# Kernel tuning notes

Measured on AMD Instinct MI355X. Metric: run time of the kernel, lower is better.

Reference implementation:

```python
import jax, jax.numpy as jnp
import numpy as np
import math

N, D, H = 4096, 2048, 16
HD = D // H  # head_dim = 128


def setup_inputs() -> dict:
    key = jax.random.key(0)
    ks = jax.random.split(key, 9)
    s = 1.0 / math.sqrt(D)
    return {
        "x":  jax.random.normal(ks[0], (N, D), dtype=jnp.float32),
        "Wq": jax.random.normal(ks[1], (D, D), dtype=jnp.float32) * s,
        "bq": jax.random.normal(ks[2], (D,), dtype=jnp.float32) * s,
        "Wk": jax.random.normal(ks[3], (D, D), dtype=jnp.float32) * s,
        "bk": jax.random.normal(ks[4], (D,), dtype=jnp.float32) * s,
        "Wv": jax.random.normal(ks[5], (D, D), dtype=jnp.float32) * s,
        "bv": jax.random.normal(ks[6], (D,), dtype=jnp.float32) * s,
        "Wo": jax.random.normal(ks[7], (D, D), dtype=jnp.float32) * s,
        "bo": jax.random.normal(ks[8], (D,), dtype=jnp.float32) * s,
    }


def reference(x, Wq, bq, Wk, bk, Wv, bv, Wo, bo):
    # eqx.nn.Linear: y = W @ x + b, weight shape (out, in) -> x @ W.T + b
    q = x @ Wq.T + bq            # [N, D]
    k = x @ Wk.T + bk            # [N, D]
    v = x @ Wv.T + bv            # [N, D]
    q = q.reshape(N, H, HD).transpose(1, 0, 2)   # [H, N, hd]
    k = k.reshape(N, H, HD).transpose(1, 2, 0)   # [H, hd, N]
    v = v.reshape(N, H, HD).transpose(1, 0, 2)   # [H, N, hd]
    scale = 1.0 / math.sqrt(HD)
    scores = jnp.matmul(q * scale, k)            # [H, N, N]
    attn = jax.nn.softmax(scores, axis=-1)
    ctx = jnp.matmul(attn, v)                    # [H, N, hd]
    ctx = ctx.transpose(1, 0, 2).reshape(N, D)   # [N, D]
    return ctx @ Wo.T + bo
```

## Files before the change

kernel.cpp:

```cpp
#include <hip/hip_runtime.h>
#include <stdint.h>

#define N_TOK 4096
#define DIM   2048
#define NH    16
#define HD    128
#define NW    (DIM * DIM)

using bf16x8 = __attribute__((ext_vector_type(8))) short;
using bf16x4 = __attribute__((ext_vector_type(4))) short;
using f32x4  = __attribute__((ext_vector_type(4))) float;
using u32x2  = __attribute__((ext_vector_type(2))) unsigned int;

#if __has_builtin(__builtin_amdgcn_exp2f)
#define EXP2(x) __builtin_amdgcn_exp2f(x)
#else
#define EXP2(x) exp2f(x)
#endif

__device__ inline unsigned short f2bf(float f) {
  union { float f; unsigned u; } v; v.f = f;
  unsigned r = v.u + 0x7FFFu + ((v.u >> 16) & 1u);
  return (unsigned short)(r >> 16);
}
__device__ inline float bf2f(unsigned short u) {
  union { unsigned u; float f; } v; v.u = ((unsigned)u) << 16; return v.f;
}
__device__ inline f32x4 mfma16(bf16x8 a, bf16x8 b, f32x4 c) {
  return __builtin_amdgcn_mfma_f32_16x16x32_bf16(a, b, c, 0, 0, 0);
}
__device__ inline void gll16(const unsigned short* g, unsigned short* l) {
  __builtin_amdgcn_global_load_lds(
      (const __attribute__((address_space(1))) void*)g,
      (__attribute__((address_space(3))) void*)l, 16, 0, 0);
}
__device__ inline void wgbar() {
  asm volatile("" ::: "memory");
  __builtin_amdgcn_s_barrier();
  asm volatile("" ::: "memory");
}

__device__ inline unsigned cvtpk_bf16(float lo, float hi) {
  unsigned r;
  asm("v_cvt_pk_bf16_f32 %0, %1, %2" : "=v"(r) : "v"(lo), "v"(hi));
  return r;
}

__device__ inline u32x2 pl32swap(unsigned a, unsigned b) {
#if __has_builtin(__builtin_amdgcn_permlane32_swap)
  return __builtin_amdgcn_permlane32_swap(a, b, false, false);
#else
  int lane = threadIdx.x & 63;
  unsigned as = (unsigned)__shfl_xor((int)a, 32);
  unsigned bs = (unsigned)__shfl_xor((int)b, 32);
  u32x2 r;
  r.x = (lane & 32) ? bs : a;
  r.y = (lane & 32) ? b : as;
  return r;
#endif
}
__device__ inline u32x2 pl16swap(unsigned a, unsigned b) {
#if __has_builtin(__builtin_amdgcn_permlane16_swap)
  return __builtin_amdgcn_permlane16_swap(a, b, false, false);
#else
  int lane = threadIdx.x & 63;
  unsigned as = (unsigned)__shfl_xor((int)a, 16);
  unsigned bs = (unsigned)__shfl_xor((int)b, 16);
  u32x2 r;
  r.x = (lane & 16) ? bs : a;
  r.y = (lane & 16) ? b : as;
  return r;
#endif
}

__global__ __launch_bounds__(256)
void cvt_bf16(const float* __restrict__ src, unsigned short* __restrict__ dst, int n) {
  int i = blockIdx.x * 256 + threadIdx.x;
  if (i * 8 >= n) return;
  const float4* s = (const float4*)src + (size_t)i * 2;
  float4 a = s[0], b = s[1];
  bf16x8 o;
  o[0] = (short)f2bf(a.x); o[1] = (short)f2bf(a.y);
  o[2] = (short)f2bf(a.z); o[3] = (short)f2bf(a.w);
  o[4] = (short)f2bf(b.x); o[5] = (short)f2bf(b.y);
  o[6] = (short)f2bf(b.z); o[7] = (short)f2bf(b.w);
  *(bf16x8*)(dst + (size_t)i * 8) = o;
}

template<int OUT_MODE>
__global__ __launch_bounds__(512, 2)
void gemm_bf16(const unsigned short* __restrict__ A, const unsigned short* __restrict__ B,
               const float* __restrict__ bias, void* __restrict__ out_, float scale) {
  constexpr int BM = 256, BN = 128, BK = 64;
  constexpr int NKT = DIM / BK;
  __shared__ unsigned short Asl[3][BM * BK];
  __shared__ unsigned short Bsl[3][BN * BK];

  const int tid  = threadIdx.x;
  const int lane = tid & 63;
  const int w    = tid >> 6;
  const int wm = w >> 1, wn = w & 1;
  const int lr = lane & 15, quad = lane >> 4;

  const int bid = blockIdx.x;
  const int nb  = (bid & 7) * 32 + (bid >> 3);
  const int m0  = (nb >> 4) * BM;
  const int n0  = (nb & 15) * BN;

  const f32x4 vzero = {0.f, 0.f, 0.f, 0.f};
  f32x4 acc[4][4];
#pragma unroll
  for (int i = 0; i < 4; ++i)
#pragma unroll
    for (int j = 0; j < 4; ++j) acc[i][j] = vzero;

  size_t asrc[4]; int aldst[4];
  size_t bsrc[2]; int bldst[2];
#pragma unroll
  for (int i = 0; i < 4; ++i) {
    int ch = tid + i * 512;
    int row = ch >> 3, cc = ch & 7;
    int gcc = cc ^ (row & 7);
    asrc[i]  = (size_t)(m0 + row) * DIM + gcc * 8;
    aldst[i] = ch * 8;
  }
#pragma unroll
  for (int i = 0; i < 2; ++i) {
    int ch = tid + i * 512;
    int row = ch >> 3, cc = ch & 7;
    int gcc = cc ^ (row & 7);
    bsrc[i]  = (size_t)(n0 + row) * DIM + gcc * 8;
    bldst[i] = ch * 8;
  }
  auto stage_half = [&](int buf, int k0, int half) {
    int a0 = half * 2;
    gll16(&A[asrc[a0] + k0],     &Asl[buf][aldst[a0]]);
    gll16(&A[asrc[a0 + 1] + k0], &Asl[buf][aldst[a0 + 1]]);
    gll16(&B[bsrc[half] + k0],   &Bsl[buf][bldst[half]]);
  };

  auto lda = [&](int buf, int ks, bf16x8* af) {
#pragma unroll
    for (int mb = 0; mb < 4; ++mb) {
      int row  = wm * 64 + mb * 16 + lr;
      int slot = (ks * 4 + quad) ^ (row & 7);
      af[mb] = *(const bf16x8*)&Asl[buf][row * 64 + slot * 8];
    }
  };
  auto ldb = [&](int buf, int ks, bf16x8* bfv) {
#pragma unroll
    for (int nb2 = 0; nb2 < 4; ++nb2) {
      int row  = wn * 64 + nb2 * 16 + lr;
      int slot = (ks * 4 + quad) ^ (row & 7);
      bfv[nb2] = *(const bf16x8*)&Bsl[buf][row * 64 + slot * 8];
    }
  };
  auto mm = [&](bf16x8* af, bf16x8* bfv) {
    __builtin_amdgcn_s_setprio(1);
#pragma unroll
    for (int mb = 0; mb < 4; ++mb)
#pragma unroll
      for (int nb2 = 0; nb2 < 4; ++nb2)
        acc[mb][nb2] = mfma16(af[mb], bfv[nb2], acc[mb][nb2]);
    __builtin_amdgcn_s_setprio(0);
  };

  stage_half(0, 0, 0);  stage_half(0, 0, 1);
  stage_half(1, BK, 0); stage_half(1, BK, 1);
  asm volatile("s_waitcnt vmcnt(6)" ::: "memory");
  wgbar();

  for (int t = 0; t < NKT - 2; ++t) {
    const int buf = t % 3, sb = (t + 2) % 3, sk = (t + 2) * BK;
    bf16x8 af[4], bfv[4];
    lda(buf, 0, af); ldb(buf, 0, bfv);
    stage_half(sb, sk, 0);
    wgbar();
    mm(af, bfv);
    wgbar();
    lda(buf, 1, af); ldb(buf, 1, bfv);
    stage_half(sb, sk, 1);
    asm volatile("s_waitcnt vmcnt(6)" ::: "memory");
    wgbar();
    mm(af, bfv);
    wgbar();
  }
  {
    const int buf = (NKT - 2) % 3;
    bf16x8 af[4], bfv[4];
    lda(buf, 0, af); ldb(buf, 0, bfv);
    wgbar(); mm(af, bfv); wgbar();
    lda(buf, 1, af); ldb(buf, 1, bfv);
    asm volatile("s_waitcnt vmcnt(0)" ::: "memory");
    wgbar(); mm(af, bfv); wgbar();
  }
  {
    const int buf = (NKT - 1) % 3;
    bf16x8 af[4], bfv[4];
    lda(buf, 0, af); ldb(buf, 0, bfv);
    mm(af, bfv);
    lda(buf, 1, af); ldb(buf, 1, bfv);
    mm(af, bfv);
  }

#pragma unroll
  for (int mb = 0; mb < 4; ++mb)
#pragma unroll
    for (int nb2 = 0; nb2 < 4; ++nb2) {
      int gn = n0 + wn * 64 + nb2 * 16 + lr;
      int gm_base = m0 + wm * 64 + mb * 16 + quad * 4;
      float bs = bias[gn];
      if constexpr (OUT_MODE == 2) {
        bf16x4 pk;
#pragma unroll
        for (int r = 0; r < 4; ++r) pk[r] = (short)f2bf((acc[mb][nb2][r] + bs) * scale);
        *(bf16x4*)&((unsigned short*)out_)[(size_t)gn * N_TOK + gm_base] = pk;
      } else {
#pragma unroll
        for (int r = 0; r < 4; ++r) {
          float v = (acc[mb][nb2][r] + bs) * scale;
          if constexpr (OUT_MODE == 1)
            ((float*)out_)[(size_t)(gm_base + r) * DIM + gn] = v;
          else
            ((unsigned short*)out_)[(size_t)(gm_base + r) * DIM + gn] = f2bf(v);
        }
      }
    }
}

__global__ __launch_bounds__(256, 1)
void flash_attn(const unsigned short* __restrict__ Q,
                const unsigned short* __restrict__ K,
                const unsigned short* __restrict__ Vt,
                unsigned short* __restrict__ ctx) {
  constexpr int LDK = 136;
  constexpr int LDV = 72;
  constexpr int NT  = N_TOK / 64;
  __shared__ unsigned short Ksl[64 * LDK];
  __shared__ unsigned short VTsl[128 * LDV];

  const int tid  = threadIdx.x;
  const int lane = tid & 63, w = tid >> 6;
  const int lr = lane & 15, quad = lane >> 4;

  const int bid  = blockIdx.x;
  const int head = (bid & 7) * 2 + ((bid >> 3) & 1);
  const int qblk = bid >> 4;
  const int hoff = head * HD;
  const int q0   = qblk * 256;
  const int qw   = q0 + w * 64;

  bf16x8 qf[4][4];
#pragma unroll
  for (int mb = 0; mb < 4; ++mb)
#pragma unroll
    for (int c = 0; c < 4; ++c)
      qf[mb][c] = *(const bf16x8*)&Q[(size_t)(qw + mb * 16 + lr) * DIM + hoff + c * 32 + quad * 8];

  const f32x4 vzero = {0.f, 0.f, 0.f, 0.f};
  f32x4 o[4][8];
  float l_acc[4] = {0.f, 0.f, 0.f, 0.f};
#pragma unroll
  for (int mb = 0; mb < 4; ++mb)
#pragma unroll
    for (int nb = 0; nb < 8; ++nb) o[mb][nb] = vzero;

  bf16x8 kreg[4], vreg[4];
  auto load_tile = [&](int kt) {
    int kbase = kt * 64;
#pragma unroll
    for (int i = 0; i < 4; ++i) {
      int ch = tid + i * 256;
      kreg[i] = *(const bf16x8*)&K[(size_t)(kbase + (ch >> 4)) * DIM + hoff + (ch & 15) * 8];
      vreg[i] = *(const bf16x8*)&Vt[(size_t)(hoff + (ch >> 3)) * N_TOK + kbase + (ch & 7) * 8];
    }
  };
  load_tile(0);

  for (int kt = 0; kt < NT; ++kt) {
    __syncthreads();
#pragma unroll
    for (int i = 0; i < 4; ++i) {
      int ch = tid + i * 256;
      *(bf16x8*)&Ksl[(ch >> 4) * LDK + (ch & 15) * 8] = kreg[i];
      *(bf16x8*)&VTsl[(ch >> 3) * LDV + (ch & 7) * 8] = vreg[i];
    }
    __syncthreads();
    if (kt + 1 < NT) load_tile(kt + 1);

    f32x4 s[4][4];
#pragma unroll
    for (int mb = 0; mb < 4; ++mb)
#pragma unroll
      for (int nf = 0; nf < 4; ++nf) s[mb][nf] = vzero;
#pragma unroll
    for (int nf = 0; nf < 4; ++nf)
#pragma unroll
      for (int c = 0; c < 4; ++c) {
        bf16x8 kf = *(const bf16x8*)&Ksl[(nf * 16 + lr) * LDK + c * 32 + quad * 8];
#pragma unroll
        for (int mb = 0; mb < 4; ++mb) s[mb][nf] = mfma16(kf, qf[mb][c], s[mb][nf]);
      }

    bf16x8 pf[4][2];
#pragma unroll
    for (int mb = 0; mb < 4; ++mb) {
      unsigned W[4][2];
      float lp = 0.f;
#pragma unroll
      for (int nf = 0; nf < 4; ++nf) {
        float e0 = EXP2(s[mb][nf][0]);
        float e1 = EXP2(s[mb][nf][1]);
        float e2 = EXP2(s[mb][nf][2]);
        float e3 = EXP2(s[mb][nf][3]);
        lp += (e0 + e1) + (e2 + e3);
        W[nf][0] = cvtpk_bf16(e0, e1);
        W[nf][1] = cvtpk_bf16(e2, e3);
      }
      l_acc[mb] += lp;
#pragma unroll
      for (int ki = 0; ki < 2; ++ki) {
        u32x2 a0  = pl32swap(W[2 * ki][0], W[2 * ki + 1][0]);
        u32x2 t02 = pl16swap(a0.x, a0.y);
        u32x2 a1  = pl32swap(W[2 * ki][1], W[2 * ki + 1][1]);
        u32x2 t13 = pl16swap(a1.x, a1.y);
        union { unsigned u[4]; bf16x8 v; } pu;
        pu.u[0] = t02.x; pu.u[1] = t13.x; pu.u[2] = t02.y; pu.u[3] = t13.y;
        pf[mb][ki] = pu.v;
      }
    }

#pragma unroll
    for (int nb = 0; nb < 8; ++nb)
#pragma unroll
      for (int ki = 0; ki < 2; ++ki) {
        bf16x8 vf = *(const bf16x8*)&VTsl[(nb * 16 + lr) * LDV + ki * 32 + quad * 8];
#pragma unroll
        for (int mb = 0; mb < 4; ++mb) o[mb][nb] = mfma16(pf[mb][ki], vf, o[mb][nb]);
      }
  }

#pragma unroll
  for (int mb = 0; mb < 4; ++mb) {
    float t = l_acc[mb];
    t += __shfl_xor(t, 16);
    t += __shfl_xor(t, 32);
    l_acc[mb] = t;
  }
#pragma unroll
  for (int mb = 0; mb < 4; ++mb)
#pragma unroll
    for (int r = 0; r < 4; ++r) {
      float Lr = __shfl(l_acc[mb], quad * 4 + r);
      float inv = 1.0f / Lr;
      int gq = qw + mb * 16 + quad * 4 + r;
#pragma unroll
      for (int nb = 0; nb < 8; ++nb)
        ctx[(size_t)gq * DIM + hoff + nb * 16 + lr] = f2bf(o[mb][nb][r] * inv);
    }
}

extern "C" void kernel_launch(void* const* d_in, const int* in_sizes, int n_in,
                              void* d_out, int out_size, void* d_ws, size_t ws_size,
                              hipStream_t stream) {
  (void)in_sizes; (void)n_in; (void)out_size; (void)ws_size;
  const float* x  = (const float*)d_in[0];
  const float* Wq = (const float*)d_in[1];
  const float* bq = (const float*)d_in[2];
  const float* Wk = (const float*)d_in[3];
  const float* bk = (const float*)d_in[4];
  const float* Wv = (const float*)d_in[5];
  const float* bv = (const float*)d_in[6];
  const float* Wo = (const float*)d_in[7];
  const float* bo = (const float*)d_in[8];

  const size_t NE = (size_t)N_TOK * DIM;
  unsigned short* xb  = (unsigned short*)d_ws;
  unsigned short* Wqb = xb + NE;
  unsigned short* Wkb = Wqb + NW;
  unsigned short* Wvb = Wkb + NW;
  unsigned short* Wob = Wvb + NW;
  unsigned short* Qb  = Wob + NW;
  unsigned short* Kb  = Qb + NE;
  unsigned short* Vtb = Kb + NE;

  cvt_bf16<<<4096, 256, 0, stream>>>(x,  xb,  (int)NE);
  cvt_bf16<<<2048, 256, 0, stream>>>(Wq, Wqb, NW);
  cvt_bf16<<<2048, 256, 0, stream>>>(Wk, Wkb, NW);
  cvt_bf16<<<2048, 256, 0, stream>>>(Wv, Wvb, NW);
  cvt_bf16<<<2048, 256, 0, stream>>>(Wo, Wob, NW);

  const float qscale = 1.4426950408889634f * 0.08838834764831845f;

  gemm_bf16<0><<<256, 512, 0, stream>>>(xb, Wqb, bq, Qb, qscale);
  gemm_bf16<0><<<256, 512, 0, stream>>>(xb, Wkb, bk, Kb, 1.0f);
  gemm_bf16<2><<<256, 512, 0, stream>>>(xb, Wvb, bv, Vtb, 1.0f);

  unsigned short* ctxb = xb;
  flash_attn<<<256, 256, 0, stream>>>(Qb, Kb, Vtb, ctxb);

  gemm_bf16<1><<<256, 512, 0, stream>>>(ctxb, Wob, bo, (float*)d_out, 1.0f);
}
```

Measured before the change: 436.3 us.

## Split GEMM main loop into quarter-steps interleaving half-A loads with MFMAs

Restructures the projection GEMM's K-loop so each half-K step is split into two sub-steps, each loading only half of the A fragments and issuing 8 MFMAs instead of 16. Global-to-LDS staging is spread as A-pair and B-half pieces across four phases. The intent is to cut register pressure for A fragments and interleave LDS reads, global loads and MFMA work more finely. In exchange it doubles the number of workgroup barriers per iteration, which may add sync overhead.

```diff
diff --git a/kernel.cpp b/kernel.cpp
--- a/kernel.cpp
+++ b/kernel.cpp
@@ -132,19 +132,20 @@
     bsrc[i]  = (size_t)(n0 + row) * DIM + gcc * 8;
     bldst[i] = ch * 8;
   }
-  auto stage_half = [&](int buf, int k0, int half) {
-    int a0 = half * 2;
-    gll16(&A[asrc[a0] + k0],     &Asl[buf][aldst[a0]]);
-    gll16(&A[asrc[a0 + 1] + k0], &Asl[buf][aldst[a0 + 1]]);
-    gll16(&B[bsrc[half] + k0],   &Bsl[buf][bldst[half]]);
+  auto stage_a = [&](int buf, int k0, int pair) {
+    gll16(&A[asrc[pair * 2] + k0],     &Asl[buf][aldst[pair * 2]]);
+    gll16(&A[asrc[pair * 2 + 1] + k0], &Asl[buf][aldst[pair * 2 + 1]]);
   };
-
-  auto lda = [&](int buf, int ks, bf16x8* af) {
-#pragma unroll
-    for (int mb = 0; mb < 4; ++mb) {
-      int row  = wm * 64 + mb * 16 + lr;
+  auto stage_b = [&](int buf, int k0, int half) {
+    gll16(&B[bsrc[half] + k0], &Bsl[buf][bldst[half]]);
+  };
+
+  auto lda2 = [&](int buf, int ks, int mbh, bf16x8* af2) {
+#pragma unroll
+    for (int i = 0; i < 2; ++i) {
+      int row  = wm * 64 + (mbh * 2 + i) * 16 + lr;
       int slot = (ks * 4 + quad) ^ (row & 7);
-      af[mb] = *(const bf16x8*)&Asl[buf][row * 64 + slot * 8];
+      af2[i] = *(const bf16x8*)&Asl[buf][row * 64 + slot * 8];
     }
   };
   auto ldb = [&](int buf, int ks, bf16x8* bfv) {
@@ -155,53 +156,62 @@
       bfv[nb2] = *(const bf16x8*)&Bsl[buf][row * 64 + slot * 8];
     }
   };
-  auto mm = [&](bf16x8* af, bf16x8* bfv) {
-    __builtin_amdgcn_s_setprio(1);
-#pragma unroll
-    for (int mb = 0; mb < 4; ++mb)
-#pragma unroll
-      for (int nb2 = 0; nb2 < 4; ++nb2)
-        acc[mb][nb2] = mfma16(af[mb], bfv[nb2], acc[mb][nb2]);
-    __builtin_amdgcn_s_setprio(0);
-  };
-
-  stage_half(0, 0, 0);  stage_half(0, 0, 1);
-  stage_half(1, BK, 0); stage_half(1, BK, 1);
+
+#define MMH(MB0)                                                          \
+  do {                                                                    \
+    __builtin_amdgcn_s_setprio(1);                                        \
+    _Pragma("unroll")                                                     \
+    for (int i_ = 0; i_ < 2; ++i_)                                        \
+      _Pragma("unroll")                                                   \
+      for (int n_ = 0; n_ < 4; ++n_)                                      \
+        acc[(MB0) + i_][n_] = mfma16(af2[i_], bfv[n_], acc[(MB0) + i_][n_]); \
+    __builtin_amdgcn_s_setprio(0);                                        \
+  } while (0)
+
+  stage_a(0, 0, 0);  stage_a(0, 0, 1);  stage_b(0, 0, 0);  stage_b(0, 0, 1);
+  stage_a(1, BK, 0); stage_a(1, BK, 1); stage_b(1, BK, 0); stage_b(1, BK, 1);
   asm volatile("s_waitcnt vmcnt(6)" ::: "memory");
   wgbar();
 
   for (int t = 0; t < NKT - 2; ++t) {
     const int buf = t % 3, sb = (t + 2) % 3, sk = (t + 2) * BK;
-    bf16x8 af[4], bfv[4];
-    lda(buf, 0, af); ldb(buf, 0, bfv);
-    stage_half(sb, sk, 0);
-    wgbar();
-    mm(af, bfv);
-    wgbar();
-    lda(buf, 1, af); ldb(buf, 1, bfv);
-    stage_half(sb, sk, 1);
+    bf16x8 af2[2], bfv[4];
+    ldb(buf, 0, bfv); lda2(buf, 0, 0, af2);
+    stage_a(sb, sk, 0);
+    wgbar(); MMH(0); wgbar();
+    lda2(buf, 0, 1, af2);
+    stage_b(sb, sk, 0);
+    wgbar(); MMH(2); wgbar();
+    ldb(buf, 1, bfv); lda2(buf, 1, 0, af2);
+    stage_a(sb, sk, 1);
+    wgbar(); MMH(0); wgbar();
+    lda2(buf, 1, 1, af2);
+    stage_b(sb, sk, 1);
     asm volatile("s_waitcnt vmcnt(6)" ::: "memory");
-    wgbar();
-    mm(af, bfv);
-    wgbar();
+    wgbar(); MMH(2); wgbar();
   }
   {
     const int buf = (NKT - 2) % 3;
-    bf16x8 af[4], bfv[4];
-    lda(buf, 0, af); ldb(buf, 0, bfv);
-    wgbar(); mm(af, bfv); wgbar();
-    lda(buf, 1, af); ldb(buf, 1, bfv);
+    bf16x8 af2[2], bfv[4];
+    ldb(buf, 0, bfv); lda2(buf, 0, 0, af2);
+    wgbar(); MMH(0); wgbar();
+    lda2(buf, 0, 1, af2);
+    wgbar(); MMH(2); wgbar();
+    ldb(buf, 1, bfv); lda2(buf, 1, 0, af2);
+    wgbar(); MMH(0); wgbar();
+    lda2(buf, 1, 1, af2);
     asm volatile("s_waitcnt vmcnt(0)" ::: "memory");
-    wgbar(); mm(af, bfv); wgbar();
+    wgbar(); MMH(2); wgbar();
   }
   {
     const int buf = (NKT - 1) % 3;
-    bf16x8 af[4], bfv[4];
-    lda(buf, 0, af); ldb(buf, 0, bfv);
-    mm(af, bfv);
-    lda(buf, 1, af); ldb(buf, 1, bfv);
-    mm(af, bfv);
-  }
+    bf16x8 af2[2], bfv[4];
+    ldb(buf, 0, bfv); lda2(buf, 0, 0, af2); MMH(0);
+    lda2(buf, 0, 1, af2);                   MMH(2);
+    ldb(buf, 1, bfv); lda2(buf, 1, 0, af2); MMH(0);
+    lda2(buf, 1, 1, af2);                   MMH(2);
+  }
+#undef MMH
 
 #pragma unroll
   for (int mb = 0; mb < 4; ++mb)
```

Result: slower. 504.8 us (+15.7%).
